# Kernel optimization log

Hardware: AMD Instinct MI355X
Metric: run time of the kernel (lower is better)

The kernel has to match this reference:

```python
import jax, jax.numpy as jnp
import numpy as np

N = 200000      # total nodes
NG = 100000     # masked (graph) nodes
NU = N - NG     # unconnected nodes
E = 3200000     # edges (index into graph nodes)
C = 1000000     # candidate pairs


def setup_inputs() -> dict:
    key = jax.random.key(0)
    ks = jax.random.split(key, 16)
    s = 0.1  # weight init scale
    x = jax.random.normal(ks[0], (N, 2), jnp.float32)
    mask = jnp.arange(N) < NG
    candidates = jnp.stack([
        jax.random.randint(ks[1], (C,), 0, NG),
        jax.random.randint(ks[2], (C,), 0, NU),
    ], axis=1).astype(jnp.int32)
    edges = jax.random.randint(ks[3], (2, E), 0, NG).astype(jnp.int32)
    return {
        "x": x, "mask": mask, "candidates": candidates, "edges": edges,
        # GraphConv(2,8): lin_rel on aggregated neighbors, lin_root on self, bias in rel
        "w1_rel": jax.random.normal(ks[4], (2, 8), jnp.float32) * s,
        "w1_root": jax.random.normal(ks[5], (2, 8), jnp.float32) * s,
        "b1": jnp.zeros((8,), jnp.float32),
        # GraphConv(8,16)
        "w2_rel": jax.random.normal(ks[6], (8, 16), jnp.float32) * s,
        "w2_root": jax.random.normal(ks[7], (8, 16), jnp.float32) * s,
        "b2": jnp.zeros((16,), jnp.float32),
        # fc_unconnected: Linear(2,16) (source's Linear(8,16) is inconsistent with 2-dim x)
        "wu": jax.random.normal(ks[8], (2, 16), jnp.float32) * s,
        "bu": jnp.zeros((16,), jnp.float32),
        # fc: Linear(32,64) -> ReLU -> Linear(64,1)
        "wa": jax.random.normal(ks[9], (32, 64), jnp.float32) * s,
        "ba": jnp.zeros((64,), jnp.float32),
        "wb": jax.random.normal(ks[10], (64, 1), jnp.float32) * s,
        "bb": jnp.zeros((1,), jnp.float32),
    }


def graph_conv(h, edges, w_rel, w_root, b, n):
    # PyG GraphConv with aggr='add': out_i = W_rel @ sum_{j->i} h_j + W_root @ h_i + b
    src, dst = edges[0], edges[1]
    agg = jax.ops.segment_sum(h[src], dst, num_segments=n)  # [n, d_in]
    return agg @ w_rel + h @ w_root + b


def reference(x, mask, candidates, edges, w1_rel, w1_root, b1,
              w2_rel, w2_root, b2, wu, bu, wa, ba, wb, bb):
    idx_g = jnp.nonzero(mask, size=NG)[0]      # graph node indices
    idx_u = jnp.nonzero(~mask, size=NU)[0]     # unconnected node indices
    x_unconnected = x[idx_u] @ wu + bu                         # [NU, 16]
    h = jax.nn.relu(graph_conv(x[idx_g], edges, w1_rel, w1_root, b1, NG))  # [NG, 8]
    h = jax.nn.relu(graph_conv(h, edges, w2_rel, w2_root, b2, NG))         # [NG, 16]
    ec = jnp.concatenate([h[candidates[:, 0]], x_unconnected[candidates[:, 1]]], axis=-1)  # [C, 32]
    hid = jax.nn.relu(ec @ wa + ba)            # [C, 64]
    return jnp.squeeze(hid @ wb + bb, -1)      # [C]
```

## Files before the change

### kernel.cpp

```cpp
#include <hip/hip_runtime.h>

#define N_TOT  200000
#define NG_    100000
#define NU_    100000
#define E_CNT  3200000
#define C_CNT  1000000

#define NBUCK  196
#define NBLK   256
#define CHUNK  12500

__global__ __launch_bounds__(256) void phaseA(const int* __restrict__ dst,
                                              int* __restrict__ cnt_mat) {
    __shared__ int hcnt[NBUCK];
    int t = threadIdx.x;
    if (t < NBUCK) hcnt[t] = 0;
    __syncthreads();
    int beg = blockIdx.x * CHUNK, end = beg + CHUNK;
    for (int e = beg + t; e < end; e += 256)
        atomicAdd(&hcnt[dst[e] >> 9], 1);
    __syncthreads();
    if (t < NBUCK) cnt_mat[blockIdx.x * NBUCK + t] = hcnt[t];
}

__global__ __launch_bounds__(256) void phaseB1(const int* __restrict__ cnt_mat,
                                               int* __restrict__ off_mat,
                                               int* __restrict__ colsum) {
    __shared__ int s[256];
    int t = threadIdx.x;
    int k = blockIdx.x;
    int v = cnt_mat[t * NBUCK + k];
    s[t] = v;
    __syncthreads();
    for (int off = 1; off < 256; off <<= 1) {
        int u = (t >= off) ? s[t - off] : 0;
        __syncthreads();
        s[t] += u;
        __syncthreads();
    }
    off_mat[t * NBUCK + k] = s[t] - v;
    if (t == 255) colsum[k] = s[255];
}

__global__ __launch_bounds__(256) void phaseB2(const int* __restrict__ colsum,
                                               int* __restrict__ bbase) {
    __shared__ int s[256];
    int t = threadIdx.x;
    int v = (t < NBUCK) ? colsum[t] : 0;
    s[t] = v;
    __syncthreads();
    for (int off = 1; off < 256; off <<= 1) {
        int u = (t >= off) ? s[t - off] : 0;
        __syncthreads();
        s[t] += u;
        __syncthreads();
    }
    if (t < NBUCK) bbase[t] = s[t] - v;
    if (t == NBUCK - 1) bbase[NBUCK] = s[t];
}

__global__ __launch_bounds__(256) void phaseC(const int* __restrict__ src,
                                              const int* __restrict__ dst,
                                              const int* __restrict__ off_mat,
                                              const int* __restrict__ bbase,
                                              int* __restrict__ pairs) {
    __shared__ int loc[NBUCK];
    int t = threadIdx.x;
    if (t < NBUCK) loc[t] = bbase[t] + off_mat[blockIdx.x * NBUCK + t];
    __syncthreads();
    int beg = blockIdx.x * CHUNK, end = beg + CHUNK;
    for (int e = beg + t; e < end; e += 256) {
        int d = dst[e], s = src[e];
        int k = d >> 9;
        int pos = atomicAdd(&loc[k], 1);
        pairs[pos] = (s << 9) | (d & 511);
    }
}

__global__ __launch_bounds__(1024) void phaseD(const int* __restrict__ bbase,
                                               const int* __restrict__ pairs,
                                               int* __restrict__ csr_src,
                                               int* __restrict__ node_off) {
    __shared__ int cnt[512], scn[512], base[512];
    int t = threadIdx.x, k = blockIdx.x;
    if (t < 512) cnt[t] = 0;
    __syncthreads();
    int beg = bbase[k], end = bbase[k + 1];
    for (int e = beg + t; e < end; e += 1024)
        atomicAdd(&cnt[pairs[e] & 511], 1);
    __syncthreads();
    if (t < 512) scn[t] = cnt[t];
    __syncthreads();
    for (int off = 1; off < 512; off <<= 1) {
        int v = 0;
        if (t < 512 && t >= off) v = scn[t - off];
        __syncthreads();
        if (t < 512) scn[t] += v;
        __syncthreads();
    }
    if (t < 512) {
        int bse = beg + scn[t] - cnt[t];
        base[t] = bse;
        node_off[(k << 9) + t] = bse;
    }
    __syncthreads();
    for (int e = beg + t; e < end; e += 1024) {
        int p = pairs[e];
        int pos = atomicAdd(&base[p & 511], 1);
        csr_src[pos] = p >> 9;
    }
}

__global__ __launch_bounds__(256) void conv1_csr(const int* __restrict__ node_off,
                                                 const int* __restrict__ csr_src,
                                                 const float* __restrict__ x,
                                                 const float* __restrict__ w_rel,
                                                 const float* __restrict__ w_root,
                                                 const float* __restrict__ b,
                                                 float* __restrict__ h1) {
    int t = threadIdx.x;
    int n = blockIdx.x * 32 + (t >> 3);
    int l = t & 7;
    int beg = node_off[n], end = node_off[n + 1];
    float a0 = 0.f, a1 = 0.f;
    for (int e = beg + l; e < end; e += 8) {
        int s = csr_src[e];
        float2 xv = *(const float2*)(x + 2 * s);
        a0 += xv.x; a1 += xv.y;
    }
#pragma unroll
    for (int d = 1; d < 8; d <<= 1) {
        a0 += __shfl_xor(a0, d, 64);
        a1 += __shfl_xor(a1, d, 64);
    }
    float2 xn = *(const float2*)(x + 2 * n);
    float v = a0 * w_rel[l] + a1 * w_rel[8 + l]
            + xn.x * w_root[l] + xn.y * w_root[8 + l] + b[l];
    h1[8 * n + l] = fmaxf(v, 0.f);
}

__global__ __launch_bounds__(256) void conv2_csr(const int* __restrict__ node_off,
                                                 const int* __restrict__ csr_src,
                                                 const float* __restrict__ h1,
                                                 const float* __restrict__ w_rel,
                                                 const float* __restrict__ w_root,
                                                 const float* __restrict__ b,
                                                 float* __restrict__ h2) {
    int t = threadIdx.x;
    int n = blockIdx.x * 32 + (t >> 3);
    int l = t & 7;
    int beg = node_off[n], end = node_off[n + 1];
    float acc[8] = {0.f, 0.f, 0.f, 0.f, 0.f, 0.f, 0.f, 0.f};
    for (int e = beg + l; e < end; e += 8) {
        int s = csr_src[e];
        const float4* hp = (const float4*)(h1 + 8 * s);
        float4 v0 = hp[0], v1 = hp[1];
        acc[0] += v0.x; acc[1] += v0.y; acc[2] += v0.z; acc[3] += v0.w;
        acc[4] += v1.x; acc[5] += v1.y; acc[6] += v1.z; acc[7] += v1.w;
    }
#pragma unroll
    for (int d = 1; d < 8; d <<= 1)
#pragma unroll
        for (int j = 0; j < 8; j++)
            acc[j] += __shfl_xor(acc[j], d, 64);
    const float4* hp = (const float4*)(h1 + 8 * n);
    float4 t0 = hp[0], t1 = hp[1];
    float hn[8] = {t0.x, t0.y, t0.z, t0.w, t1.x, t1.y, t1.z, t1.w};
#pragma unroll
    for (int cc = 0; cc < 2; cc++) {
        int c = l + 8 * cc;
        float v = b[c];
#pragma unroll
        for (int j = 0; j < 8; j++)
            v += acc[j] * w_rel[j * 16 + c] + hn[j] * w_root[j * 16 + c];
        h2[16 * n + c] = fmaxf(v, 0.f);
    }
}

__global__ void prep_kernel(const float* __restrict__ wu,
                            const float* __restrict__ bu,
                            const float* __restrict__ wa,
                            const float* __restrict__ ba,
                            float* __restrict__ wprep) {
    int j = threadIdx.x;
#pragma unroll
    for (int i = 0; i < 16; i++) wprep[j * 16 + i] = wa[i * 64 + j];
    float c0 = 0.f, c1 = 0.f, bc = ba[j];
#pragma unroll
    for (int k = 0; k < 16; k++) {
        float w = wa[(16 + k) * 64 + j];
        c0 += wu[k] * w;
        c1 += wu[16 + k] * w;
        bc += bu[k] * w;
    }
    wprep[1024 + j] = c0;
    wprep[1088 + j] = c1;
    wprep[1152 + j] = bc;
}

__global__ __launch_bounds__(256) void final_mlp2(const int* __restrict__ cand,
                                                  const float* __restrict__ h2,
                                                  const float* __restrict__ x,
                                                  const float* __restrict__ wprep,
                                                  const float* __restrict__ wb,
                                                  const float* __restrict__ bb,
                                                  float* __restrict__ out) {
    int c = blockIdx.x * 256 + threadIdx.x;
    if (c >= C_CNT) return;
    int g = cand[2 * c], u = cand[2 * c + 1];
    float ec[16];
    const float4* hp = (const float4*)(h2 + 16 * g);
#pragma unroll
    for (int q = 0; q < 4; q++) {
        float4 v = hp[q];
        ec[4 * q] = v.x; ec[4 * q + 1] = v.y; ec[4 * q + 2] = v.z; ec[4 * q + 3] = v.w;
    }
    float2 xv = *(const float2*)(x + 2 * (NG_ + u));
    float acc = bb[0];
#pragma unroll 4
    for (int j = 0; j < 64; j++) {
        float v = wprep[1152 + j] + xv.x * wprep[1024 + j] + xv.y * wprep[1088 + j];
        const float* wr = wprep + j * 16;
#pragma unroll
        for (int i = 0; i < 16; i++) v += ec[i] * wr[i];
        acc += fmaxf(v, 0.f) * wb[j];
    }
    out[c] = acc;
}


extern "C" void kernel_launch(void* const* d_in, const int* in_sizes, int n_in,
                              void* d_out, int out_size, void* d_ws, size_t ws_size,
                              hipStream_t stream) {
    const float* x      = (const float*)d_in[0];
    const int*   cand   = (const int*)d_in[2];
    const int*   edges  = (const int*)d_in[3];
    const float* w1_rel = (const float*)d_in[4];
    const float* w1_root= (const float*)d_in[5];
    const float* b1     = (const float*)d_in[6];
    const float* w2_rel = (const float*)d_in[7];
    const float* w2_root= (const float*)d_in[8];
    const float* b2     = (const float*)d_in[9];
    const float* wu     = (const float*)d_in[10];
    const float* bu     = (const float*)d_in[11];
    const float* wa     = (const float*)d_in[12];
    const float* ba     = (const float*)d_in[13];
    const float* wb     = (const float*)d_in[14];
    const float* bb     = (const float*)d_in[15];
    float* out = (float*)d_out;

    const int* src = edges;
    const int* dst = edges + E_CNT;

    int* ws_i = (int*)d_ws;
    int*   cnt_mat  = ws_i;
    int*   off_mat  = ws_i + 50176;
    int*   colsum   = ws_i + 100352;
    int*   bbase    = ws_i + 100608;
    int*   node_off = ws_i + 100864;
    float* wprep    = (float*)(ws_i + 201728);
    int*   pairs    = ws_i + 202944;
    int*   csr_src  = ws_i + 3402944;
    float* h1       = (float*)(ws_i + 6602944);
    float* h2       = (float*)(ws_i + 7402944);

    dim3 blk256(256);

    prep_kernel<<<1, 64, 0, stream>>>(wu, bu, wa, ba, wprep);
    phaseA <<<NBLK, blk256, 0, stream>>>(dst, cnt_mat);
    phaseB1<<<NBUCK, blk256, 0, stream>>>(cnt_mat, off_mat, colsum);
    phaseB2<<<1, blk256, 0, stream>>>(colsum, bbase);
    phaseC <<<NBLK, blk256, 0, stream>>>(src, dst, off_mat, bbase, pairs);
    phaseD <<<NBUCK, 1024, 0, stream>>>(bbase, pairs, csr_src, node_off);
    conv1_csr<<<3125, blk256, 0, stream>>>(node_off, csr_src, x, w1_rel, w1_root, b1, h1);
    conv2_csr<<<3125, blk256, 0, stream>>>(node_off, csr_src, h1, w2_rel, w2_root, b2, h2);
    final_mlp2<<<(C_CNT + 255) / 256, blk256, 0, stream>>>(cand, h2, x, wprep, wb, bb, out);
}
```

Measured before the change: 266.0 us.

## Precompute per-graph-node first MLP layer projection before candidate gather

Adds a kernel that computes, for each of the graph nodes, the 64-wide product of h2 with the first fc weight rows plus the folded bias, and stores it in reused workspace (the old pairs buffer). The candidate kernel then gathers 64 precomputed floats per candidate instead of doing a 16x64 matvec, which removes about a million redundant matvecs. In exchange each candidate's gather grows from 64 to 256 bytes, and an extra 25.6 MB buffer is written and read back.

```diff
diff --git a/kernel.cpp b/kernel.cpp
--- a/kernel.cpp
+++ b/kernel.cpp
@@ -198,8 +198,41 @@
     wprep[1152 + j] = bc;
 }
 
-__global__ __launch_bounds__(256) void final_mlp2(const int* __restrict__ cand,
-                                                  const float* __restrict__ h2,
+__global__ __launch_bounds__(256) void precompA(const float* __restrict__ h2,
+                                                const float* __restrict__ wa,
+                                                const float* __restrict__ wprep,
+                                                float* __restrict__ Ag) {
+    int g = blockIdx.x * 256 + threadIdx.x;
+    if (g >= NG_) return;
+    float h[16];
+    const float4* hp = (const float4*)(h2 + 16 * g);
+#pragma unroll
+    for (int q = 0; q < 4; q++) {
+        float4 v = hp[q];
+        h[4*q] = v.x; h[4*q+1] = v.y; h[4*q+2] = v.z; h[4*q+3] = v.w;
+    }
+    float4* op = (float4*)(Ag + 64 * g);
+#pragma unroll
+    for (int q = 0; q < 16; q++) {
+        float4 v;
+        v.x = wprep[1152 + 4*q + 0];
+        v.y = wprep[1152 + 4*q + 1];
+        v.z = wprep[1152 + 4*q + 2];
+        v.w = wprep[1152 + 4*q + 3];
+#pragma unroll
+        for (int i = 0; i < 16; i++) {
+            float hi = h[i];
+            v.x += hi * wa[i*64 + 4*q + 0];
+            v.y += hi * wa[i*64 + 4*q + 1];
+            v.z += hi * wa[i*64 + 4*q + 2];
+            v.w += hi * wa[i*64 + 4*q + 3];
+        }
+        op[q] = v;
+    }
+}
+
+__global__ __launch_bounds__(256) void final_mlp3(const int* __restrict__ cand,
+                                                  const float* __restrict__ Ag,
                                                   const float* __restrict__ x,
                                                   const float* __restrict__ wprep,
                                                   const float* __restrict__ wb,
@@ -208,22 +241,20 @@
     int c = blockIdx.x * 256 + threadIdx.x;
     if (c >= C_CNT) return;
     int g = cand[2 * c], u = cand[2 * c + 1];
-    float ec[16];
-    const float4* hp = (const float4*)(h2 + 16 * g);
-#pragma unroll
-    for (int q = 0; q < 4; q++) {
-        float4 v = hp[q];
-        ec[4 * q] = v.x; ec[4 * q + 1] = v.y; ec[4 * q + 2] = v.z; ec[4 * q + 3] = v.w;
-    }
     float2 xv = *(const float2*)(x + 2 * (NG_ + u));
+    const float4* ap = (const float4*)(Ag + 64 * g);
     float acc = bb[0];
-#pragma unroll 4
-    for (int j = 0; j < 64; j++) {
-        float v = wprep[1152 + j] + xv.x * wprep[1024 + j] + xv.y * wprep[1088 + j];
-        const float* wr = wprep + j * 16;
-#pragma unroll
-        for (int i = 0; i < 16; i++) v += ec[i] * wr[i];
-        acc += fmaxf(v, 0.f) * wb[j];
+#pragma unroll
+    for (int q = 0; q < 16; q++) {
+        float4 a = ap[q];
+        float v0 = a.x + xv.x * wprep[1024 + 4*q + 0] + xv.y * wprep[1088 + 4*q + 0];
+        float v1 = a.y + xv.x * wprep[1024 + 4*q + 1] + xv.y * wprep[1088 + 4*q + 1];
+        float v2 = a.z + xv.x * wprep[1024 + 4*q + 2] + xv.y * wprep[1088 + 4*q + 2];
+        float v3 = a.w + xv.x * wprep[1024 + 4*q + 3] + xv.y * wprep[1088 + 4*q + 3];
+        acc += fmaxf(v0, 0.f) * wb[4*q + 0];
+        acc += fmaxf(v1, 0.f) * wb[4*q + 1];
+        acc += fmaxf(v2, 0.f) * wb[4*q + 2];
+        acc += fmaxf(v3, 0.f) * wb[4*q + 3];
     }
     out[c] = acc;
 }
@@ -263,6 +294,7 @@
     int*   csr_src  = ws_i + 3402944;
     float* h1       = (float*)(ws_i + 6602944);
     float* h2       = (float*)(ws_i + 7402944);
+    float* Ag       = (float*)(ws_i + 202944);
 
     dim3 blk256(256);
 
@@ -274,5 +306,6 @@
     phaseD <<<NBUCK, 1024, 0, stream>>>(bbase, pairs, csr_src, node_off);
     conv1_csr<<<3125, blk256, 0, stream>>>(node_off, csr_src, x, w1_rel, w1_root, b1, h1);
     conv2_csr<<<3125, blk256, 0, stream>>>(node_off, csr_src, h1, w2_rel, w2_root, b2, h2);
-    final_mlp2<<<(C_CNT + 255) / 256, blk256, 0, stream>>>(cand, h2, x, wprep, wb, bb, out);
-}
+    precompA<<<(NG_ + 255) / 256, blk256, 0, stream>>>(h2, wa, wprep, Ag);
+    final_mlp3<<<(C_CNT + 255) / 256, blk256, 0, stream>>>(cand, Ag, x, wprep, wb, bb, out);
+}
```

Result: slower. 275.1 us (+3.4%).
